# Optimization experiments

Measured on AMD Instinct MI355X. Metric: run time of the kernel, lower is better.

## Reference

```python
import jax, jax.numpy as jnp
import numpy as np

NUM_HEADS = 12

def quick_gelu(z):
    return z * jax.nn.sigmoid(1.702 * z)

def setup_inputs() -> dict:
    key = jax.random.key(0)
    ks = jax.random.split(key, 8)
    B, Fn, P, E, R = 16, 12, 197, 768, 8
    s = 0.02
    return {
        "x": jax.random.normal(ks[0], (B * Fn, P, E), jnp.float32),
        "in_proj_weight": jax.random.normal(ks[1], (3 * E, E), jnp.float32) * s,
        "in_proj_bias": jnp.zeros((3 * E,), jnp.float32),
        "out_proj_weight": jax.random.normal(ks[2], (E, E), jnp.float32) * s,
        "out_proj_bias": jnp.zeros((E,), jnp.float32),
        "lora_a": jax.random.normal(ks[3], (R, E), jnp.float32) * s,
        "lora_b": jax.random.normal(ks[4], (3 * E, R), jnp.float32) * s,
        "down_w": jax.random.normal(ks[5], (R, E), jnp.float32) * s,
        "down_b": jnp.zeros((R,), jnp.float32),
        "up_w": jax.random.normal(ks[6], (E, R), jnp.float32) * s,
        "up_b": jnp.zeros((E,), jnp.float32),
        "b": B, "n_f": Fn, "token_len": P, "d_v": E,
    }

def reference(x, in_proj_weight, in_proj_bias, out_proj_weight, out_proj_bias,
              lora_a, lora_b, down_w, down_b, up_w, up_b,
              b, n_f, token_len, d_v):
    bsz, tgt, E = x.shape
    h = NUM_HEADS
    hd = E // h
    scaling = float(hd) ** -0.5

    # fused qkv + LoRA delta: [bsz, tgt, 3E]
    qkv = x @ in_proj_weight.T + in_proj_bias
    qkv = qkv + (x @ lora_a.T) @ lora_b.T
    qkv = qkv.reshape(bsz, tgt, 3, h, hd).transpose(2, 0, 3, 1, 4)
    q, k, v = qkv[0], qkv[1], qkv[2]  # each [bsz, h, tgt, hd]

    # CLS-token query per frame: (b f) h p d -> b h f d  (p=0)
    q_1 = q.reshape(b, n_f, h, tgt, hd).transpose(0, 2, 1, 3, 4)[:, :, :, 0, :]

    # per-frame local attention
    attn = jax.nn.softmax((scaling * q) @ k.transpose(0, 1, 3, 2), axis=-1)
    out = (attn @ v).transpose(0, 2, 1, 3).reshape(bsz, tgt, E)
    out = out @ out_proj_weight.T + out_proj_bias

    # cross-frame kv: (b f) h p d -> b h (f p) d
    k_all = k.reshape(b, n_f, h, tgt, hd).transpose(0, 2, 1, 3, 4).reshape(b, h, n_f * tgt, hd)
    v_all = v.reshape(b, n_f, h, tgt, hd).transpose(0, 2, 1, 3, 4).reshape(b, h, n_f * tgt, hd)

    attn_1 = jax.nn.softmax((scaling * q_1) @ k_all.transpose(0, 1, 3, 2), axis=-1)
    x_1 = (attn_1 @ v_all).transpose(0, 2, 1, 3).reshape(b, n_f, E)
    x_1 = x_1 @ out_proj_weight.T + out_proj_bias

    out = out.reshape(b, n_f, token_len, d_v)
    x_0 = out[:, :, 0, :]
    x_0 = quick_gelu(x_0 @ down_w.T + down_b) @ up_w.T + up_b
    out = out.at[:, :, 0, :].set(x_0 + x_1)
    return out.reshape(b * n_f, token_len, d_v)
```

## Files before the change

kernel.cpp:

```cpp
#include <hip/hip_runtime.h>
#include <hip/hip_bf16.h>

typedef __hip_bfloat16 bf16;
typedef __attribute__((ext_vector_type(8))) short bf16x8;
typedef __attribute__((ext_vector_type(4))) float f32x4;

#define NT   37824
#define MPAD 37888
#define EDIM 768
#define N3   2304
#define TP   197
#define NB   16
#define NF   12
#define NH   12
#define HD   64
#define SCALE 0.125f
#define KALL 2364

__device__ __forceinline__ float bits2f(unsigned short u) {
    unsigned int v = ((unsigned int)u) << 16;
    return __uint_as_float(v);
}
__device__ __forceinline__ float b2f(bf16 v) { return __bfloat162float(v); }

__device__ __forceinline__ unsigned short bhi(float x) {
    union { bf16 b; unsigned short u; } cv; cv.b = __float2bfloat16(x); return cv.u;
}
__device__ __forceinline__ unsigned short blo(float x, unsigned short h) {
    float hf = __uint_as_float(((unsigned int)h) << 16);
    union { bf16 b; unsigned short u; } cv; cv.b = __float2bfloat16(x - hf); return cv.u;
}

__device__ __forceinline__ void storeC(float* p, float v) { *p = v; }
__device__ __forceinline__ void storeC(bf16* p, float v) { *p = __float2bfloat16(v); }

__device__ __forceinline__ void gload_lds16(const bf16* g, bf16* l) {
    __builtin_amdgcn_global_load_lds(
        (const __attribute__((address_space(1))) void*)g,
        (__attribute__((address_space(3))) void*)l,
        16, 0, 0);
}

__global__ __launch_bounds__(256) void lora_mid_kernel(const float* __restrict__ x,
        const float* __restrict__ la, float* __restrict__ mid) {
    int t = blockIdx.x * 4 + (threadIdx.x >> 6);
    int lane = threadIdx.x & 63;
    if (t >= NT) return;
    float acc[8];
#pragma unroll
    for (int r = 0; r < 8; r++) acc[r] = 0.f;
    const float* xr = x + (size_t)t * EDIM;
    for (int e = lane; e < EDIM; e += 64) {
        float xv = xr[e];
#pragma unroll
        for (int r = 0; r < 8; r++) acc[r] += xv * la[r * EDIM + e];
    }
#pragma unroll
    for (int r = 0; r < 8; r++) {
        float v = acc[r];
#pragma unroll
        for (int off = 32; off >= 1; off >>= 1) v += __shfl_xor(v, off, 64);
        if (lane == 0) mid[(size_t)t * 8 + r] = v;
    }
}

__global__ __launch_bounds__(256) void split_w_kernel(const float* __restrict__ w,
        bf16* __restrict__ o, int rows) {
    int idx = blockIdx.x * 256 + threadIdx.x;
    int total = rows * 192;
    if (idx >= total) return;
    int r = idx / 192, c = (idx - r * 192) * 4;
    float4 v = *reinterpret_cast<const float4*>(w + (size_t)r * 768 + c);
    ushort4 hi, lo;
    hi.x = bhi(v.x); hi.y = bhi(v.y); hi.z = bhi(v.z); hi.w = bhi(v.w);
    lo.x = blo(v.x, hi.x); lo.y = blo(v.y, hi.y); lo.z = blo(v.z, hi.z); lo.w = blo(v.w, hi.w);
    *(ushort4*)(o + (size_t)r * 1536 + c) = hi;
    *(ushort4*)(o + (size_t)r * 1536 + 768 + c) = lo;
}

template <typename OT, bool LORA>
__global__ __launch_bounds__(512, 2) void mfma_gemm_kernel(const bf16* __restrict__ A, int lda,
        const bf16* __restrict__ W, const float* __restrict__ bias,
        const float* __restrict__ mid, const float* __restrict__ lb,
        OT* __restrict__ C, int M, int N, int KV) {
    __shared__ bf16 As[2][256 * 64];
    __shared__ bf16 Bs[2][256 * 64];
    const int tid = threadIdx.x;
    const int w = tid >> 6, lane = tid & 63;
    const int lr = lane & 15, lg = lane >> 4;
    const int wr = w >> 2, wc = w & 3;

    const int gx = gridDim.x;
    const int nwg = gx * gridDim.y;
    const int flat = blockIdx.y * gx + blockIdx.x;
    const int xcd = flat & 7, loc = flat >> 3;
    const int q = nwg >> 3, rmd = nwg & 7;
    const int lid = (xcd < rmd ? xcd * (q + 1) : rmd * (q + 1) + (xcd - rmd) * q) + loc;
    const int m0 = (lid / gx) * 256, n0 = (lid % gx) * 256;

    f32x4 acc[8][4];
#pragma unroll
    for (int i = 0; i < 8; i++)
#pragma unroll
        for (int j = 0; j < 4; j++) acc[i][j] = (f32x4){0.f, 0.f, 0.f, 0.f};

    const int brs = lane >> 3;
    const int bcsw = ((lane & 7) ^ brs) << 3;

    auto STAGE = [&](bf16* dA, bf16* dB, int aO, int wO) {
#pragma unroll
        for (int j = 0; j < 4; ++j) {
            int rA = w * 32 + j * 8;
            gload_lds16(A + (size_t)(m0 + rA + brs) * lda + aO + bcsw, dA + rA * 64);
            gload_lds16(W + (size_t)(n0 + rA + brs) * 1536 + wO + bcsw, dB + rA * 64);
        }
    };

    const int nt = KV / 64;
    STAGE(&As[0][0], &Bs[0][0], 0, 0);
    {
        const int k1 = 64;
        STAGE(&As[1][0], &Bs[1][0], (k1 >= 768) ? k1 - 768 : k1, k1);
    }
    asm volatile("s_waitcnt vmcnt(8)" ::: "memory");
    __builtin_amdgcn_sched_barrier(0);
    __builtin_amdgcn_s_barrier();
    __builtin_amdgcn_sched_barrier(0);

    int cur = 0;
    for (int t = 0; t < nt; ++t) {
        const char* pA = (const char*)&As[cur][0];
        const char* pB = (const char*)&Bs[cur][0];
        bf16x8 a[4][2], b[4][2];
#pragma unroll
        for (int nf = 0; nf < 4; nf++) {
            int row = wc * 64 + nf * 16 + lr;
            int sw = (row & 7) << 4;
            b[nf][0] = *(const bf16x8*)(pB + row * 128 + ((lg * 16) ^ sw));
            b[nf][1] = *(const bf16x8*)(pB + row * 128 + ((64 + lg * 16) ^ sw));
        }
#pragma unroll
        for (int mf = 0; mf < 4; mf++) {
            int row = wr * 128 + mf * 16 + lr;
            int sw = (row & 7) << 4;
            a[mf][0] = *(const bf16x8*)(pA + row * 128 + ((lg * 16) ^ sw));
            a[mf][1] = *(const bf16x8*)(pA + row * 128 + ((64 + lg * 16) ^ sw));
        }
        __builtin_amdgcn_s_setprio(1);
#pragma unroll
        for (int mf = 0; mf < 4; mf++)
#pragma unroll
            for (int nf = 0; nf < 4; nf++) {
                acc[mf][nf] = __builtin_amdgcn_mfma_f32_16x16x32_bf16(a[mf][0], b[nf][0], acc[mf][nf], 0, 0, 0);
                acc[mf][nf] = __builtin_amdgcn_mfma_f32_16x16x32_bf16(a[mf][1], b[nf][1], acc[mf][nf], 0, 0, 0);
            }
        __builtin_amdgcn_s_setprio(0);
        __builtin_amdgcn_sched_barrier(0);
        __builtin_amdgcn_s_barrier();
        __builtin_amdgcn_sched_barrier(0);
#pragma unroll
        for (int mf = 0; mf < 4; mf++) {
            int row = wr * 128 + 64 + mf * 16 + lr;
            int sw = (row & 7) << 4;
            a[mf][0] = *(const bf16x8*)(pA + row * 128 + ((lg * 16) ^ sw));
            a[mf][1] = *(const bf16x8*)(pA + row * 128 + ((64 + lg * 16) ^ sw));
        }
        __builtin_amdgcn_s_setprio(1);
#pragma unroll
        for (int mf = 0; mf < 4; mf++)
#pragma unroll
            for (int nf = 0; nf < 4; nf++) {
                acc[4 + mf][nf] = __builtin_amdgcn_mfma_f32_16x16x32_bf16(a[mf][0], b[nf][0], acc[4 + mf][nf], 0, 0, 0);
                acc[4 + mf][nf] = __builtin_amdgcn_mfma_f32_16x16x32_bf16(a[mf][1], b[nf][1], acc[4 + mf][nf], 0, 0, 0);
            }
        __builtin_amdgcn_s_setprio(0);
        __builtin_amdgcn_sched_barrier(0);
        __builtin_amdgcn_s_barrier();
        __builtin_amdgcn_sched_barrier(0);
        if (t + 2 < nt) {
            const int k2 = (t + 2) * 64;
            STAGE(&As[cur][0], &Bs[cur][0],
                  (k2 >= 768) ? k2 - 768 : k2,
                  (k2 >= 1536) ? k2 - 1536 : k2);
            asm volatile("s_waitcnt vmcnt(8)" ::: "memory");
        } else {
            asm volatile("s_waitcnt vmcnt(0)" ::: "memory");
        }
        __builtin_amdgcn_sched_barrier(0);
        __builtin_amdgcn_s_barrier();
        __builtin_amdgcn_sched_barrier(0);
        cur ^= 1;
    }
#pragma unroll
    for (int mf = 0; mf < 8; mf++) {
#pragma unroll
        for (int r = 0; r < 4; r++) {
            int m = m0 + wr * 128 + mf * 16 + lg * 4 + r;
            if (m < M) {
                float mr[8];
                if constexpr (LORA) {
                    float4 u0 = *reinterpret_cast<const float4*>(mid + (size_t)m * 8);
                    float4 u1 = *reinterpret_cast<const float4*>(mid + (size_t)m * 8 + 4);
                    mr[0] = u0.x; mr[1] = u0.y; mr[2] = u0.z; mr[3] = u0.w;
                    mr[4] = u1.x; mr[5] = u1.y; mr[6] = u1.z; mr[7] = u1.w;
                }
#pragma unroll
                for (int nf = 0; nf < 4; nf++) {
                    int n = n0 + wc * 64 + nf * 16 + lr;
                    float v = acc[mf][nf][r] + bias[n];
                    if constexpr (LORA) {
                        const float4 l0 = *reinterpret_cast<const float4*>(lb + (size_t)n * 8);
                        const float4 l1 = *reinterpret_cast<const float4*>(lb + (size_t)n * 8 + 4);
                        v += mr[0] * l0.x + mr[1] * l0.y + mr[2] * l0.z + mr[3] * l0.w
                           + mr[4] * l1.x + mr[5] * l1.y + mr[6] * l1.z + mr[7] * l1.w;
                    }
                    storeC(C + (size_t)m * N + n, v);
                }
            }
        }
    }
}

__global__ __launch_bounds__(256) void attn_kernel(const bf16* __restrict__ qkv,
        bf16* __restrict__ ao) {
    __shared__ bf16 Ks[208 * 64];
    __shared__ bf16 Vt[64 * 208];
    __shared__ bf16 Ps[4][16 * 208];
    const int bb = blockIdx.x / NH;
    const int h = blockIdx.x % NH;
    const bf16* base = qkv + (size_t)bb * TP * N3;
    const int tid = threadIdx.x;
    const int w = tid >> 6, lane = tid & 63;
    const int lr = lane & 15, lg = lane >> 4;

    for (int idx = tid; idx < 208 * 16; idx += 256) {
        int row = idx >> 4, d4 = (idx & 15) * 4;
        ushort4 v = make_ushort4(0, 0, 0, 0);
        if (row < TP)
            v = *(const ushort4*)(base + (size_t)row * N3 + EDIM + h * 64 + d4);
        *(ushort4*)((char*)Ks + ((row * 128 + d4 * 2) ^ ((row & 7) << 4))) = v;
    }
    for (int g = w; g < 52; g += 4) {
        int kk0 = g * 4;
        int d = lane;
        const bf16* vb = base + (size_t)kk0 * N3 + 2 * EDIM + h * 64 + d;
        unsigned short t0 = 0, t1 = 0, t2 = 0, t3 = 0;
        if (kk0 + 0 < TP) t0 = *(const unsigned short*)(vb);
        if (kk0 + 1 < TP) t1 = *(const unsigned short*)(vb + N3);
        if (kk0 + 2 < TP) t2 = *(const unsigned short*)(vb + 2 * N3);
        if (kk0 + 3 < TP) t3 = *(const unsigned short*)(vb + 3 * N3);
        ushort4 v; v.x = t0; v.y = t1; v.z = t2; v.w = t3;
        *(ushort4*)((char*)Vt + ((d * 416 + kk0 * 2) ^ ((d & 7) << 4))) = v;
    }
    __syncthreads();

    bf16* Pw = &Ps[w][0];

    for (int qt = w; qt < 13; qt += 4) {
        int q = qt * 16 + lr; if (q > TP - 1) q = TP - 1;
        const bf16* qp = base + (size_t)q * N3 + h * 64 + lg * 8;
        bf16x8 qa0 = *(const bf16x8*)qp;
        bf16x8 qa1 = *(const bf16x8*)(qp + 32);

        f32x4 sf[13];
#pragma unroll
        for (int f = 0; f < 13; f++) {
            int row = f * 16 + lr;
            int swz = (row & 7) << 4;
            bf16x8 kb0 = *(const bf16x8*)((const char*)Ks + ((row * 128 + lg * 16) ^ swz));
            bf16x8 kb1 = *(const bf16x8*)((const char*)Ks + ((row * 128 + 64 + lg * 16) ^ swz));
            f32x4 c = {0.f, 0.f, 0.f, 0.f};
            c = __builtin_amdgcn_mfma_f32_16x16x32_bf16(qa0, kb0, c, 0, 0, 0);
            c = __builtin_amdgcn_mfma_f32_16x16x32_bf16(qa1, kb1, c, 0, 0, 0);
            sf[f] = c;
        }

        float mx[4] = {-1e30f, -1e30f, -1e30f, -1e30f};
#pragma unroll
        for (int f = 0; f < 13; f++) {
#pragma unroll
            for (int r = 0; r < 4; r++) {
                float s = sf[f][r] * SCALE;
                if (f == 12 && lr >= 5) s = -1e30f;
                sf[f][r] = s;
                mx[r] = fmaxf(mx[r], s);
            }
        }
#pragma unroll
        for (int off = 8; off >= 1; off >>= 1) {
#pragma unroll
            for (int r = 0; r < 4; r++) mx[r] = fmaxf(mx[r], __shfl_xor(mx[r], off, 64));
        }
        float lsum[4] = {0.f, 0.f, 0.f, 0.f};
#pragma unroll
        for (int f = 0; f < 13; f++) {
#pragma unroll
            for (int r = 0; r < 4; r++) {
                float e = __expf(sf[f][r] - mx[r]);
                sf[f][r] = e;
                lsum[r] += e;
            }
        }
#pragma unroll
        for (int off = 8; off >= 1; off >>= 1) {
#pragma unroll
            for (int r = 0; r < 4; r++) lsum[r] += __shfl_xor(lsum[r], off, 64);
        }
        float inv[4];
#pragma unroll
        for (int r = 0; r < 4; r++) inv[r] = 1.f / lsum[r];

#pragma unroll
        for (int f = 0; f < 13; f++) {
#pragma unroll
            for (int r = 0; r < 4; r++) {
                int row = lg * 4 + r;
                int col = f * 16 + lr;
                *(bf16*)((char*)Pw + ((row * 416 + col * 2) ^ ((row & 7) << 4))) =
                    __float2bfloat16(sf[f][r]);
            }
        }

        f32x4 of[4];
#pragma unroll
        for (int dt = 0; dt < 4; dt++) of[dt] = (f32x4){0.f, 0.f, 0.f, 0.f};
#pragma unroll
        for (int ks = 0; ks < 7; ks++) {
            int k0 = ks * 32 + lg * 8;
            bool ok = (k0 < 208);
            bf16x8 pa = {0, 0, 0, 0, 0, 0, 0, 0};
            if (ok)
                pa = *(const bf16x8*)((const char*)Pw + ((lr * 416 + k0 * 2) ^ ((lr & 7) << 4)));
#pragma unroll
            for (int dt = 0; dt < 4; dt++) {
                bf16x8 vb = {0, 0, 0, 0, 0, 0, 0, 0};
                if (ok) {
                    int d = dt * 16 + lr;
                    vb = *(const bf16x8*)((const char*)Vt + ((d * 416 + k0 * 2) ^ ((d & 7) << 4)));
                }
                of[dt] = __builtin_amdgcn_mfma_f32_16x16x32_bf16(pa, vb, of[dt], 0, 0, 0);
            }
        }

#pragma unroll
        for (int dt = 0; dt < 4; dt++) {
#pragma unroll
            for (int r = 0; r < 4; r++) {
                int qq = qt * 16 + lg * 4 + r;
                if (qq < TP)
                    ao[((size_t)bb * TP + qq) * EDIM + h * 64 + dt * 16 + lr] =
                        __float2bfloat16(of[dt][r] * inv[r]);
            }
        }
    }
}

__global__ __launch_bounds__(256) void xattn_kernel(const bf16* __restrict__ qkv,
        float* __restrict__ x1p) {
    __shared__ float q1[NF][64];
    __shared__ bf16 Ks[128][64];
    __shared__ bf16 Vs[128][64];
    __shared__ float sc[NF][128];
    __shared__ float Oacc[NF][64];
    __shared__ float mrow[NF], lrow[NF], arow[NF];
    const int b = blockIdx.x / NH, h = blockIdx.x % NH;
    const int tid = threadIdx.x;
    for (int idx = tid; idx < NF * 64; idx += 256) {
        int f = idx >> 6, d = idx & 63;
        q1[f][d] = b2f(qkv[(size_t)((b * NF + f) * TP) * N3 + h * 64 + d]);
        Oacc[f][d] = 0.f;
    }
    if (tid < NF) { mrow[tid] = -1e30f; lrow[tid] = 0.f; }
    __syncthreads();
    const int w = tid >> 6, lane = tid & 63;
    for (int kk0 = 0; kk0 < KALL; kk0 += 128) {
        for (int idx = tid; idx < 128 * 16; idx += 256) {
            int r = idx >> 4, d4 = (idx & 15) * 4;
            int kk = kk0 + r;
            if (kk < KALL) {
                int f = kk / TP, pp = kk - f * TP;
                const bf16* src = qkv + (size_t)((b * NF + f) * TP + pp) * N3 + h * 64 + d4;
                *(ushort4*)&Ks[r][d4] = *(const ushort4*)(src + 768);
                *(ushort4*)&Vs[r][d4] = *(const ushort4*)(src + 1536);
            } else {
                ushort4 z; z.x = z.y = z.z = z.w = 0;
                *(ushort4*)&Ks[r][d4] = z;
                *(ushort4*)&Vs[r][d4] = z;
            }
        }
        __syncthreads();
        for (int idx = tid; idx < NF * 128; idx += 256) {
            int f = idx >> 7, r = idx & 127;
            float s = -1e30f;
            if (kk0 + r < KALL) {
                const bf16* kr = &Ks[r][0];
                float a = 0.f;
#pragma unroll
                for (int d2 = 0; d2 < 32; d2++) {
                    unsigned int u = *reinterpret_cast<const unsigned int*>(kr + 2 * d2);
                    a += q1[f][2 * d2] * __uint_as_float(u << 16);
                    a += q1[f][2 * d2 + 1] * __uint_as_float(u & 0xffff0000u);
                }
                s = a * SCALE;
            }
            sc[f][r] = s;
        }
        __syncthreads();
        for (int qi = 0; qi < 3; qi++) {
            int f = qi * 4 + w;
            float s0 = sc[f][lane], s1v = sc[f][lane + 64];
            float mx = fmaxf(s0, s1v);
#pragma unroll
            for (int off = 32; off >= 1; off >>= 1) mx = fmaxf(mx, __shfl_xor(mx, off, 64));
            float mold = mrow[f];
            float mnew = fmaxf(mold, mx);
            float e0 = __expf(s0 - mnew), e1 = __expf(s1v - mnew);
            float ls = e0 + e1;
#pragma unroll
            for (int off = 32; off >= 1; off >>= 1) ls += __shfl_xor(ls, off, 64);
            sc[f][lane] = e0; sc[f][lane + 64] = e1;
            if (lane == 0) {
                float alpha = __expf(mold - mnew);
                arow[f] = alpha;
                lrow[f] = lrow[f] * alpha + ls;
                mrow[f] = mnew;
            }
        }
        __syncthreads();
        for (int idx = tid; idx < NF * 64; idx += 256) {
            int f = idx >> 6, d = idx & 63;
            float o = Oacc[f][d] * arow[f];
#pragma unroll 4
            for (int r = 0; r < 128; r++)
                o += sc[f][r] * b2f(Vs[r][d]);
            Oacc[f][d] = o;
        }
        __syncthreads();
    }
    for (int idx = tid; idx < NF * 64; idx += 256) {
        int f = idx >> 6, d = idx & 63;
        x1p[(size_t)(b * NF + f) * EDIM + h * 64 + d] = Oacc[f][d] / lrow[f];
    }
}

__global__ __launch_bounds__(256) void cls_kernel(float* __restrict__ out,
        const float* __restrict__ x1p, const float* __restrict__ Wout, const float* __restrict__ ob,
        const float* __restrict__ dw, const float* __restrict__ db,
        const float* __restrict__ uw, const float* __restrict__ ub) {
    __shared__ float x0s[EDIM], x1s[EDIM], gs[8];
    const int bfi = blockIdx.x;
    float* row = out + (size_t)bfi * TP * EDIM;
    const int tid = threadIdx.x;
    for (int i = tid; i < EDIM; i += 256) {
        x0s[i] = row[i];
        x1s[i] = x1p[(size_t)bfi * EDIM + i];
    }
    __syncthreads();
    {
        int r = tid >> 5, sl = tid & 31;
        float pr = 0.f;
        for (int e = sl; e < EDIM; e += 32) pr += x0s[e] * dw[r * EDIM + e];
#pragma unroll
        for (int off = 16; off >= 1; off >>= 1) pr += __shfl_xor(pr, off, 64);
        if (sl == 0) gs[r] = pr + db[r];
    }
    __syncthreads();
    float act[8];
#pragma unroll
    for (int r = 0; r < 8; r++) { float g = gs[r]; act[r] = g / (1.f + __expf(-1.702f * g)); }
    for (int j = tid; j < EDIM; j += 256) {
        float y = ub[j] + ob[j];
        const float4 u0 = *reinterpret_cast<const float4*>(uw + (size_t)j * 8);
        const float4 u1 = *reinterpret_cast<const float4*>(uw + (size_t)j * 8 + 4);
        y += act[0] * u0.x + act[1] * u0.y + act[2] * u0.z + act[3] * u0.w
           + act[4] * u1.x + act[5] * u1.y + act[6] * u1.z + act[7] * u1.w;
        const float* wr = Wout + (size_t)j * EDIM;
        float s = 0.f;
        for (int e = 0; e < EDIM; e += 4) {
            float4 wv = *reinterpret_cast<const float4*>(wr + e);
            s += x1s[e] * wv.x + x1s[e + 1] * wv.y + x1s[e + 2] * wv.z + x1s[e + 3] * wv.w;
        }
        y += s;
        row[j] = y;
    }
}

extern "C" void kernel_launch(void* const* d_in, const int* in_sizes, int n_in,
                              void* d_out, int out_size, void* d_ws, size_t ws_size,
                              hipStream_t stream) {
    (void)in_sizes; (void)n_in; (void)out_size; (void)ws_size;
    const float* x   = (const float*)d_in[0];
    const float* ipw = (const float*)d_in[1];
    const float* ipb = (const float*)d_in[2];
    const float* opw = (const float*)d_in[3];
    const float* opb = (const float*)d_in[4];
    const float* la  = (const float*)d_in[5];
    const float* lb  = (const float*)d_in[6];
    const float* dw  = (const float*)d_in[7];
    const float* db  = (const float*)d_in[8];
    const float* uw  = (const float*)d_in[9];
    const float* ub  = (const float*)d_in[10];
    float* out = (float*)d_out;

    char* wsb = (char*)d_ws;
    bf16* qkv = (bf16*)wsb;                       wsb += (size_t)NT * N3 * sizeof(bf16);
    bf16* ao  = (bf16*)wsb;                       wsb += (size_t)MPAD * EDIM * sizeof(bf16);
    bf16* xs  = (bf16*)wsb;                       wsb += (size_t)MPAD * 1536 * sizeof(bf16);
    bf16* W1  = (bf16*)wsb;                       wsb += (size_t)N3 * 1536 * sizeof(bf16);
    bf16* W2  = (bf16*)wsb;                       wsb += (size_t)EDIM * 1536 * sizeof(bf16);
    float* mid = (float*)wsb;                     wsb += (size_t)NT * 8 * sizeof(float);
    float* x1p = (float*)wsb;                     wsb += (size_t)NB * NF * EDIM * sizeof(float);

    split_w_kernel<<<(N3 * 192 + 255) / 256, 256, 0, stream>>>(ipw, W1, N3);
    split_w_kernel<<<(EDIM * 192 + 255) / 256, 256, 0, stream>>>(opw, W2, EDIM);
    split_w_kernel<<<(NT * 192 + 255) / 256, 256, 0, stream>>>(x, xs, NT);
    lora_mid_kernel<<<NT / 4, 256, 0, stream>>>(x, la, mid);
    mfma_gemm_kernel<bf16, true><<<dim3(N3 / 256, MPAD / 256), 512, 0, stream>>>(
        xs, 1536, W1, ipb, mid, lb, qkv, NT, N3, 2304);
    attn_kernel<<<192 * NH, 256, 0, stream>>>(qkv, ao);
    xattn_kernel<<<NB * NH, 256, 0, stream>>>(qkv, x1p);
    mfma_gemm_kernel<float, false><<<dim3(EDIM / 256, MPAD / 256), 512, 0, stream>>>(
        ao, 768, W2, opb, nullptr, nullptr, out, NT, EDIM, 1536);
    cls_kernel<<<NB * NF, 256, 0, stream>>>(out, x1p, opw, opb, dw, db, uw, ub);
}
```

Baseline: 1.514 ms.

## Split GEMM inner loop into quadrants and overlap global staging with MFMA

Reorders the per-tile MFMA work in the QKV GEMM main loop into four quadrants, loading B fragments in two halves so LDS reads interleave with MFMAs. One intra-iteration barrier is removed, and the last quadrant of MFMAs is issued after the next tile's global-to-LDS STAGE so the memory loads overlap compute. This aims to cut LDS-read and barrier stalls. The cost is more live registers and reliance on the remaining barriers for correctness of the double-buffered LDS reuse.

```diff
diff --git a/kernel.cpp b/kernel.cpp
--- a/kernel.cpp
+++ b/kernel.cpp
@@ -131,14 +131,7 @@
     for (int t = 0; t < nt; ++t) {
         const char* pA = (const char*)&As[cur][0];
         const char* pB = (const char*)&Bs[cur][0];
-        bf16x8 a[4][2], b[4][2];
-#pragma unroll
-        for (int nf = 0; nf < 4; nf++) {
-            int row = wc * 64 + nf * 16 + lr;
-            int sw = (row & 7) << 4;
-            b[nf][0] = *(const bf16x8*)(pB + row * 128 + ((lg * 16) ^ sw));
-            b[nf][1] = *(const bf16x8*)(pB + row * 128 + ((64 + lg * 16) ^ sw));
-        }
+        bf16x8 a[4][2], b0[2][2], b1[2][2];
 #pragma unroll
         for (int mf = 0; mf < 4; mf++) {
             int row = wr * 128 + mf * 16 + lr;
@@ -146,18 +139,38 @@
             a[mf][0] = *(const bf16x8*)(pA + row * 128 + ((lg * 16) ^ sw));
             a[mf][1] = *(const bf16x8*)(pA + row * 128 + ((64 + lg * 16) ^ sw));
         }
+#pragma unroll
+        for (int nf = 0; nf < 2; nf++) {
+            int row = wc * 64 + nf * 16 + lr;
+            int sw = (row & 7) << 4;
+            b0[nf][0] = *(const bf16x8*)(pB + row * 128 + ((lg * 16) ^ sw));
+            b0[nf][1] = *(const bf16x8*)(pB + row * 128 + ((64 + lg * 16) ^ sw));
+        }
         __builtin_amdgcn_s_setprio(1);
 #pragma unroll
         for (int mf = 0; mf < 4; mf++)
 #pragma unroll
-            for (int nf = 0; nf < 4; nf++) {
-                acc[mf][nf] = __builtin_amdgcn_mfma_f32_16x16x32_bf16(a[mf][0], b[nf][0], acc[mf][nf], 0, 0, 0);
-                acc[mf][nf] = __builtin_amdgcn_mfma_f32_16x16x32_bf16(a[mf][1], b[nf][1], acc[mf][nf], 0, 0, 0);
+            for (int nf = 0; nf < 2; nf++) {
+                acc[mf][nf] = __builtin_amdgcn_mfma_f32_16x16x32_bf16(a[mf][0], b0[nf][0], acc[mf][nf], 0, 0, 0);
+                acc[mf][nf] = __builtin_amdgcn_mfma_f32_16x16x32_bf16(a[mf][1], b0[nf][1], acc[mf][nf], 0, 0, 0);
             }
         __builtin_amdgcn_s_setprio(0);
-        __builtin_amdgcn_sched_barrier(0);
-        __builtin_amdgcn_s_barrier();
-        __builtin_amdgcn_sched_barrier(0);
+#pragma unroll
+        for (int nf = 0; nf < 2; nf++) {
+            int row = wc * 64 + (nf + 2) * 16 + lr;
+            int sw = (row & 7) << 4;
+            b1[nf][0] = *(const bf16x8*)(pB + row * 128 + ((lg * 16) ^ sw));
+            b1[nf][1] = *(const bf16x8*)(pB + row * 128 + ((64 + lg * 16) ^ sw));
+        }
+        __builtin_amdgcn_s_setprio(1);
+#pragma unroll
+        for (int mf = 0; mf < 4; mf++)
+#pragma unroll
+            for (int nf = 0; nf < 2; nf++) {
+                acc[mf][nf + 2] = __builtin_amdgcn_mfma_f32_16x16x32_bf16(a[mf][0], b1[nf][0], acc[mf][nf + 2], 0, 0, 0);
+                acc[mf][nf + 2] = __builtin_amdgcn_mfma_f32_16x16x32_bf16(a[mf][1], b1[nf][1], acc[mf][nf + 2], 0, 0, 0);
+            }
+        __builtin_amdgcn_s_setprio(0);
 #pragma unroll
         for (int mf = 0; mf < 4; mf++) {
             int row = wr * 128 + 64 + mf * 16 + lr;
@@ -169,9 +182,9 @@
 #pragma unroll
         for (int mf = 0; mf < 4; mf++)
 #pragma unroll
-            for (int nf = 0; nf < 4; nf++) {
-                acc[4 + mf][nf] = __builtin_amdgcn_mfma_f32_16x16x32_bf16(a[mf][0], b[nf][0], acc[4 + mf][nf], 0, 0, 0);
-                acc[4 + mf][nf] = __builtin_amdgcn_mfma_f32_16x16x32_bf16(a[mf][1], b[nf][1], acc[4 + mf][nf], 0, 0, 0);
+            for (int nf = 0; nf < 2; nf++) {
+                acc[4 + mf][nf + 2] = __builtin_amdgcn_mfma_f32_16x16x32_bf16(a[mf][0], b1[nf][0], acc[4 + mf][nf + 2], 0, 0, 0);
+                acc[4 + mf][nf + 2] = __builtin_amdgcn_mfma_f32_16x16x32_bf16(a[mf][1], b1[nf][1], acc[4 + mf][nf + 2], 0, 0, 0);
             }
         __builtin_amdgcn_s_setprio(0);
         __builtin_amdgcn_sched_barrier(0);
@@ -182,6 +195,18 @@
             STAGE(&As[cur][0], &Bs[cur][0],
                   (k2 >= 768) ? k2 - 768 : k2,
                   (k2 >= 1536) ? k2 - 1536 : k2);
+        }
+        __builtin_amdgcn_sched_barrier(0);
+        __builtin_amdgcn_s_setprio(1);
+#pragma unroll
+        for (int mf = 0; mf < 4; mf++)
+#pragma unroll
+            for (int nf = 0; nf < 2; nf++) {
+                acc[4 + mf][nf] = __builtin_amdgcn_mfma_f32_16x16x32_bf16(a[mf][0], b0[nf][0], acc[4 + mf][nf], 0, 0, 0);
+                acc[4 + mf][nf] = __builtin_amdgcn_mfma_f32_16x16x32_bf16(a[mf][1], b0[nf][1], acc[4 + mf][nf], 0, 0, 0);
+            }
+        __builtin_amdgcn_s_setprio(0);
+        if (t + 2 < nt) {
             asm volatile("s_waitcnt vmcnt(8)" ::: "memory");
         } else {
             asm volatile("s_waitcnt vmcnt(0)" ::: "memory");
```

Measured after the change: 1.456 ms. 3.9% less time.
